# Kernel tuning notes

Measured on AMD Instinct MI355X. Metric: run time of the kernel, lower is better.

Reference implementation:

```python
import jax, jax.numpy as jnp
import numpy as np

B, L, PD, DIM, H, DH, DEPTH, MLP, NIMG, NCLS, TH = 2, 2048, 768, 512, 8, 64, 2, 2048, 4, 1000, 32


def _ln(x, g):
    # bias-free LayerNorm (beta buffer is zeros), eps matches torch F.layer_norm
    mu = jnp.mean(x, axis=-1, keepdims=True)
    var = jnp.var(x, axis=-1, keepdims=True)
    return (x - mu) / jnp.sqrt(var + 1e-5) * g


def _rms(x, g):
    # F.normalize(dim=-1) * sqrt(dim_head) * gamma; x: [b,h,n,dh], g: [h,1,dh]
    n = jnp.linalg.norm(x, axis=-1, keepdims=True)
    return x / jnp.maximum(n, 1e-12) * (DH ** 0.5) * g


def _attn(x, context, mask, ln_g, qg, kg, Wq, Wkv, Wo):
    b, n = x.shape[0], x.shape[1]
    xn = _ln(x, ln_g)
    kv = xn if context is None else context  # context is NOT pre-normed (matches source)
    m = kv.shape[1]
    q = (xn @ Wq).reshape(b, n, H, DH).transpose(0, 2, 1, 3)   # [b,h,n,dh]
    k, v = jnp.split(kv @ Wkv, 2, axis=-1)
    k = k.reshape(b, m, H, DH).transpose(0, 2, 1, 3)
    v = v.reshape(b, m, H, DH).transpose(0, 2, 1, 3)
    q = _rms(q, qg)
    k = _rms(k, kg)
    dots = jnp.einsum('bhid,bhjd->bhij', q, k)  # no 1/sqrt(d): QK-RMSNorm carries the scale
    neg = -jnp.finfo(dots.dtype).max
    dots = jnp.where(mask, dots, neg)
    a = jax.nn.softmax(dots, axis=-1)
    out = jnp.einsum('bhij,bhjd->bhid', a, v)
    out = out.transpose(0, 2, 1, 3).reshape(b, n, H * DH)
    return out @ Wo


def _forward(patches, ln_pe1_g, W_pe, b_pe, ln_pe2_g, pos_h_emb, pos_w_emb,
             attn_ln_g, q_g, k_g, Wq, Wkv, Wo, ff_ln_g, W1, b1, W2, b2,
             final_ln_g, pool_q, pool_ln_g, pool_q_g, pool_k_g,
             pool_Wq, pool_Wkv, pool_Wo, head_ln_g, W_head,
             pos_h, pos_w, image_ids):
    # patch embedding: LN -> Linear -> LN, then factorized 2D pos embed
    x = _ln(patches, ln_pe1_g) @ W_pe + b_pe
    x = _ln(x, ln_pe2_g)
    x = x + pos_h_emb[pos_h] + pos_w_emb[pos_w]
    # block-diagonal attention mask: tokens attend only within their image
    mask = (image_ids[:, None, :, None] == image_ids[:, None, None, :])  # [B,1,L,L]
    for i in range(DEPTH):
        x = _attn(x, None, mask, attn_ln_g[i], q_g[i], k_g[i], Wq[i], Wkv[i], Wo[i]) + x
        h = _ln(x, ff_ln_g[i]) @ W1[i] + b1[i]
        h = jax.nn.gelu(h, approximate=False)
        x = h @ W2[i] + b2[i] + x
    x = _ln(x, final_ln_g)
    # attention pooling: one learned query per packed image
    queries = jnp.broadcast_to(pool_q, (B, NIMG, DIM))
    pmask = (jnp.arange(NIMG)[None, None, :, None] == image_ids[:, None, None, :])  # [B,1,NIMG,L]
    pooled = _attn(queries, x, pmask, pool_ln_g, pool_q_g, pool_k_g, pool_Wq, pool_Wkv, pool_Wo) + queries
    return _ln(pooled, head_ln_g) @ W_head  # [B, NIMG, NCLS]


def setup_inputs() -> dict:
    key = jax.random.key(0)
    ks = jax.random.split(key, 16)
    s = 0.02
    inp = {}
    inp['patches'] = jax.random.normal(ks[0], (B, L, PD), jnp.float32)
    inp['pos_h'] = jax.random.randint(ks[1], (B, L), 0, TH)
    inp['pos_w'] = jax.random.randint(ks[2], (B, L), 0, TH)
    inp['image_ids'] = jnp.sort(jax.random.randint(ks[3], (B, L), 0, NIMG), axis=-1)
    inp['ln_pe1_g'] = jnp.ones((PD,), jnp.float32)
    inp['W_pe'] = jax.random.normal(ks[4], (PD, DIM), jnp.float32) * s
    inp['b_pe'] = jnp.zeros((DIM,), jnp.float32)
    inp['ln_pe2_g'] = jnp.ones((DIM,), jnp.float32)
    inp['pos_h_emb'] = jax.random.normal(ks[5], (TH, DIM), jnp.float32)
    inp['pos_w_emb'] = jax.random.normal(ks[6], (TH, DIM), jnp.float32)
    inp['attn_ln_g'] = jnp.ones((DEPTH, DIM), jnp.float32)
    inp['q_g'] = jnp.ones((DEPTH, H, 1, DH), jnp.float32)
    inp['k_g'] = jnp.ones((DEPTH, H, 1, DH), jnp.float32)
    inp['Wq'] = jax.random.normal(ks[7], (DEPTH, DIM, H * DH), jnp.float32) * s
    inp['Wkv'] = jax.random.normal(ks[8], (DEPTH, DIM, 2 * H * DH), jnp.float32) * s
    inp['Wo'] = jax.random.normal(ks[9], (DEPTH, H * DH, DIM), jnp.float32) * s
    inp['ff_ln_g'] = jnp.ones((DEPTH, DIM), jnp.float32)
    inp['W1'] = jax.random.normal(ks[10], (DEPTH, DIM, MLP), jnp.float32) * s
    inp['b1'] = jnp.zeros((DEPTH, MLP), jnp.float32)
    inp['W2'] = jax.random.normal(ks[11], (DEPTH, MLP, DIM), jnp.float32) * s
    inp['b2'] = jnp.zeros((DEPTH, DIM), jnp.float32)
    inp['final_ln_g'] = jnp.ones((DIM,), jnp.float32)
    inp['pool_q'] = jax.random.normal(ks[12], (DIM,), jnp.float32)
    inp['pool_ln_g'] = jnp.ones((DIM,), jnp.float32)
    inp['pool_q_g'] = jnp.ones((H, 1, DH), jnp.float32)
    inp['pool_k_g'] = jnp.ones((H, 1, DH), jnp.float32)
    inp['pool_Wq'] = jax.random.normal(ks[13], (DIM, H * DH), jnp.float32) * s
    inp['pool_Wkv'] = jax.random.normal(ks[14], (DIM, 2 * H * DH), jnp.float32) * s
    inp['pool_Wo'] = jax.random.normal(ks[15], (H * DH, DIM), jnp.float32) * s
    inp['head_ln_g'] = jnp.ones((DIM,), jnp.float32)
    inp['W_head'] = jax.random.normal(jax.random.fold_in(key, 99), (DIM, NCLS), jnp.float32) * s
    return inp


def reference(patches, pos_h, pos_w, image_ids, ln_pe1_g, W_pe, b_pe, ln_pe2_g,
              pos_h_emb, pos_w_emb, attn_ln_g, q_g, k_g, Wq, Wkv, Wo, ff_ln_g,
              W1, b1, W2, b2, final_ln_g, pool_q, pool_ln_g, pool_q_g, pool_k_g,
              pool_Wq, pool_Wkv, pool_Wo, head_ln_g, W_head):
    return _forward(patches, ln_pe1_g, W_pe, b_pe, ln_pe2_g, pos_h_emb, pos_w_emb,
                    attn_ln_g, q_g, k_g, Wq, Wkv, Wo, ff_ln_g, W1, b1, W2, b2,
                    final_ln_g, pool_q, pool_ln_g, pool_q_g, pool_k_g,
                    pool_Wq, pool_Wkv, pool_Wo, head_ln_g, W_head,
                    pos_h, pos_w, image_ids)
```

## Files before the change

### kernel.cpp

```cpp
#include <hip/hip_runtime.h>
#include <hip/hip_bf16.h>
#include <cfloat>
#include <math.h>

#define BB 2
#define LL 2048
#define PD 768
#define DIM 512
#define HH 8
#define DH 64
#define DEPTH 2
#define MLP 2048
#define NIMG 4
#define NCLS 1000
#define ROWS (BB*LL)
#define QKV (3*DIM)
#define NEGBIG (-1e30f)

typedef __hip_bfloat16 bf16;
typedef __bf16 v8bf __attribute__((ext_vector_type(8)));
typedef float f32x4 __attribute__((ext_vector_type(4)));

__device__ __forceinline__ float ldin(const void* p, size_t i, int bf) {
    return bf ? __bfloat162float(((const bf16*)p)[i]) : ((const float*)p)[i];
}
__device__ __forceinline__ float lda(const float* p, size_t i) { return p[i]; }
__device__ __forceinline__ float lda(const bf16* p, size_t i) { return __bfloat162float(p[i]); }
__device__ __forceinline__ void st(float* p, size_t i, float v) { p[i] = v; }
__device__ __forceinline__ void st(bf16* p, size_t i, float v) { p[i] = __float2bfloat16(v); }
__device__ __forceinline__ unsigned short f2bf(float x) {
    return __builtin_bit_cast(unsigned short, __float2bfloat16(x));
}
__device__ __forceinline__ float us2f(unsigned short u) {
    return __bfloat162float(__builtin_bit_cast(bf16, u));
}

__device__ __forceinline__ void stage16(const void* gsrc, void* ldst)
{
    __builtin_amdgcn_global_load_lds(
        (const __attribute__((address_space(1))) unsigned int*)(unsigned long long)gsrc,
        (__attribute__((address_space(3))) unsigned int*)(unsigned int)(unsigned long long)ldst,
        16, 0, 0);
}

__global__ void detect_dtype_kernel(const void* ones, int* flag)
{
    if (threadIdx.x == 0 && blockIdx.x == 0)
        *flag = (((const unsigned*)ones)[0] == 0x3F803F80u) ? 1 : 0;
}

__global__ void wconv_kernel(const void* __restrict__ W, int K, int N, size_t inStride,
                             bf16* __restrict__ out, size_t outOff, size_t outStride,
                             const int* dtf)
{
    __shared__ float t[32][33];
    const int bf = *dtf;
    const size_t zin = (size_t)blockIdx.z * inStride;
    const size_t zout = outOff + (size_t)blockIdx.z * outStride;
    const int kb = blockIdx.y * 32, nb = blockIdx.x * 32;
    const int tx = threadIdx.x, ty = threadIdx.y;
    #pragma unroll
    for (int u = 0; u < 4; ++u)
        t[ty + 8 * u][tx] = ldin(W, zin + (size_t)(kb + ty + 8 * u) * N + nb + tx, bf);
    __syncthreads();
    #pragma unroll
    for (int u = 0; u < 4; ++u)
        out[zout + (size_t)(nb + ty + 8 * u) * K + kb + tx] = __float2bfloat16(t[tx][ty + 8 * u]);
}

template<int RAWIN, typename TOUT>
__global__ void ln_kernel(const void* __restrict__ in, const void* __restrict__ g, size_t goff,
                          TOUT* __restrict__ out, int D, const int* dtf)
{
    __shared__ float red[16];
    const int bf = *dtf;
    const int row = blockIdx.x, tid = threadIdx.x;
    const size_t base = (size_t)row * D;
    float s = 0.f, ss = 0.f;
    for (int d = tid; d < D; d += blockDim.x) {
        float v = RAWIN ? ldin(in, base + d, bf) : ((const float*)in)[base + d];
        s += v; ss += v * v;
    }
    for (int o = 32; o; o >>= 1) { s += __shfl_xor(s, o); ss += __shfl_xor(ss, o); }
    const int wid = tid >> 6, lane = tid & 63, nw = blockDim.x >> 6;
    if (lane == 0) { red[wid] = s; red[8 + wid] = ss; }
    __syncthreads();
    if (tid == 0) {
        float a = 0.f, b = 0.f;
        for (int w = 0; w < nw; ++w) { a += red[w]; b += red[8 + w]; }
        red[0] = a; red[8] = b;
    }
    __syncthreads();
    const float mean = red[0] / D;
    const float var  = red[8] / D - mean * mean;
    const float rstd = rsqrtf(var + 1e-5f);
    for (int d = tid; d < D; d += blockDim.x) {
        float v = RAWIN ? ldin(in, base + d, bf) : ((const float*)in)[base + d];
        st(out, base + d, (v - mean) * rstd * ldin(g, goff + d, bf));
    }
}

__global__ void patch_fuse_kernel(const float* __restrict__ part,
                                  const void* __restrict__ b_pe,
                                  const void* __restrict__ g1,
                                  const void* __restrict__ phe, const void* __restrict__ pwe,
                                  const int* __restrict__ ph, const int* __restrict__ pw,
                                  const void* __restrict__ g2,
                                  float* __restrict__ x, bf16* __restrict__ xb,
                                  const int* dtf)
{
    __shared__ float red[16];
    const int bf = *dtf;
    const int row = blockIdx.x, tid = threadIdx.x;
    const size_t base = (size_t)row * DIM;
    const int wid = tid >> 6, lane = tid & 63;
    float v[2];
    float s = 0.f, ss = 0.f;
    #pragma unroll
    for (int u = 0; u < 2; ++u) {
        const int d = tid + 256 * u;
        float a = part[base + d] + part[(size_t)ROWS * DIM + base + d] + ldin(b_pe, d, bf);
        v[u] = a; s += a; ss += a * a;
    }
    for (int o = 32; o; o >>= 1) { s += __shfl_xor(s, o); ss += __shfl_xor(ss, o); }
    if (lane == 0) { red[wid] = s; red[8 + wid] = ss; }
    __syncthreads();
    if (tid == 0) {
        float a = 0.f, b = 0.f;
        for (int w2 = 0; w2 < 4; ++w2) { a += red[w2]; b += red[8 + w2]; }
        red[0] = a; red[8] = b;
    }
    __syncthreads();
    {
        const float mean = red[0] / DIM;
        const float var  = red[8] / DIM - mean * mean;
        const float rstd = rsqrtf(var + 1e-5f);
        const size_t hoff = (size_t)ph[row] * DIM, woff = (size_t)pw[row] * DIM;
        s = 0.f; ss = 0.f;
        #pragma unroll
        for (int u = 0; u < 2; ++u) {
            const int d = tid + 256 * u;
            float a = (v[u] - mean) * rstd * ldin(g1, d, bf)
                    + ldin(phe, hoff + d, bf) + ldin(pwe, woff + d, bf);
            x[base + d] = a;
            v[u] = a; s += a; ss += a * a;
        }
    }
    for (int o = 32; o; o >>= 1) { s += __shfl_xor(s, o); ss += __shfl_xor(ss, o); }
    __syncthreads();
    if (lane == 0) { red[wid] = s; red[8 + wid] = ss; }
    __syncthreads();
    if (tid == 0) {
        float a = 0.f, b = 0.f;
        for (int w2 = 0; w2 < 4; ++w2) { a += red[w2]; b += red[8 + w2]; }
        red[0] = a; red[8] = b;
    }
    __syncthreads();
    const float mean = red[0] / DIM;
    const float var  = red[8] / DIM - mean * mean;
    const float rstd = rsqrtf(var + 1e-5f);
    #pragma unroll
    for (int u = 0; u < 2; ++u) {
        const int d = tid + 256 * u;
        xb[base + d] = __float2bfloat16((v[u] - mean) * rstd * ldin(g2, d, bf));
    }
}

#define GM 128
#define GN 64
#define GK 64

template<typename TO, int EPI>
__global__ void mgemm_kernel(const bf16* __restrict__ A, const bf16* __restrict__ Wt,
                             const void* __restrict__ bias, size_t boff,
                             const float* __restrict__ resid, TO* __restrict__ out,
                             int M, int N, int K, int kc, int gelu, const int* dtf)
{
    __shared__ __align__(16) unsigned short As[GM][GK];
    __shared__ __align__(16) unsigned short Bs[GN][GK];
    const int tid = threadIdx.x;
    const int w = tid >> 6, l = tid & 63, g = l >> 4, c = l & 15;
    const int wm = (w >> 1) * 64, wn = (w & 1) * 32;
    const int m0 = blockIdx.y * GM, n0 = blockIdx.x * GN;
    const int kbeg = blockIdx.z * kc, kend = kbeg + kc;
    const int lrow = l >> 3, lcol = (l & 7) * 8;

    f32x4 acc[4][2] = {};

    for (int k0 = kbeg; k0 < kend; k0 += GK) {
        __syncthreads();
        #pragma unroll
        for (int u = 0; u < 4; ++u) {
            const int rr = 32 * w + 8 * u;
            stage16(A + (size_t)(m0 + rr + lrow) * K + k0 + lcol, &As[rr][0]);
        }
        #pragma unroll
        for (int u = 0; u < 2; ++u) {
            const int rr = 16 * w + 8 * u;
            stage16(Wt + (size_t)(n0 + rr + lrow) * K + k0 + lcol, &Bs[rr][0]);
        }
        __syncthreads();
        #pragma unroll
        for (int kk = 0; kk < GK; kk += 32) {
            v8bf av[4], bv[2];
            #pragma unroll
            for (int i = 0; i < 4; ++i) av[i] = *(const v8bf*)&As[wm + i * 16 + c][kk + 8 * g];
            #pragma unroll
            for (int j = 0; j < 2; ++j) bv[j] = *(const v8bf*)&Bs[wn + j * 16 + c][kk + 8 * g];
            #pragma unroll
            for (int i = 0; i < 4; ++i)
                #pragma unroll
                for (int j = 0; j < 2; ++j)
                    acc[i][j] = __builtin_amdgcn_mfma_f32_16x16x32_bf16(av[i], bv[j], acc[i][j], 0, 0, 0);
        }
    }

    if (EPI == 0) {
        float* po = (float*)out + (size_t)blockIdx.z * M * N;
        #pragma unroll
        for (int i = 0; i < 4; ++i) {
            const int rb = m0 + wm + i * 16 + 4 * g;
            #pragma unroll
            for (int j = 0; j < 2; ++j) {
                const int col = n0 + wn + j * 16 + c;
                #pragma unroll
                for (int r = 0; r < 4; ++r)
                    po[(size_t)(rb + r) * N + col] = acc[i][j][r];
            }
        }
    } else {
        const int bf = *dtf;
        #pragma unroll
        for (int i = 0; i < 4; ++i) {
            const int rb = m0 + wm + i * 16 + 4 * g;
            #pragma unroll
            for (int j = 0; j < 2; ++j) {
                const int col = n0 + wn + j * 16 + c;
                const float bvl = bias ? ldin(bias, boff + col, bf) : 0.f;
                #pragma unroll
                for (int r = 0; r < 4; ++r) {
                    float v = acc[i][j][r] + bvl;
                    if (gelu) v = 0.5f * v * (1.f + erff(v * 0.70710678118654752f));
                    if (resid) v += resid[(size_t)(rb + r) * N + col];
                    st(out, (size_t)(rb + r) * N + col, v);
                }
            }
        }
    }
}

__global__ void comb_ln_kernel(const float* __restrict__ part, int S,
                               const void* __restrict__ bias, size_t boff,
                               float* __restrict__ x, const void* __restrict__ g, size_t goff,
                               bf16* __restrict__ xb, const int* dtf)
{
    __shared__ float red[16];
    const int bf = *dtf;
    const int row = blockIdx.x, tid = threadIdx.x;
    const size_t base = (size_t)row * DIM;
    float v[2];
    float s = 0.f, ss = 0.f;
    #pragma unroll
    for (int u = 0; u < 2; ++u) {
        const int d = tid + 256 * u;
        float a = 0.f;
        for (int sc = 0; sc < S; ++sc) a += part[(size_t)sc * ROWS * DIM + base + d];
        if (bias) a += ldin(bias, boff + d, bf);
        a += x[base + d];
        x[base + d] = a;
        v[u] = a; s += a; ss += a * a;
    }
    for (int o = 32; o; o >>= 1) { s += __shfl_xor(s, o); ss += __shfl_xor(ss, o); }
    const int wid = tid >> 6, lane = tid & 63;
    if (lane == 0) { red[wid] = s; red[8 + wid] = ss; }
    __syncthreads();
    if (tid == 0) {
        float a = 0.f, b = 0.f;
        for (int w2 = 0; w2 < 4; ++w2) { a += red[w2]; b += red[8 + w2]; }
        red[0] = a; red[8] = b;
    }
    __syncthreads();
    const float mean = red[0] / DIM;
    const float var  = red[8] / DIM - mean * mean;
    const float rstd = rsqrtf(var + 1e-5f);
    #pragma unroll
    for (int u = 0; u < 2; ++u) {
        const int d = tid + 256 * u;
        xb[base + d] = __float2bfloat16((v[u] - mean) * rstd * ldin(g, goff + d, bf));
    }
}

#define TS 16
template<typename TA, typename TO>
__global__ void gemm_kernel(const TA* __restrict__ A, const void* __restrict__ W, size_t woff,
                            const void* __restrict__ bias, size_t boff,
                            const float* __restrict__ resid, TO* __restrict__ out,
                            int M, int N, int K, int gelu, const int* dtf)
{
    __shared__ float As[TS][TS + 1];
    __shared__ float Bs[TS][TS + 1];
    const int bf = *dtf;
    const int tx = threadIdx.x, ty = threadIdx.y;
    const int col = blockIdx.x * TS + tx;
    const int row = blockIdx.y * TS + ty;
    float acc = 0.f;
    for (int k0 = 0; k0 < K; k0 += TS) {
        const int ka = k0 + tx;
        As[ty][tx] = (row < M && ka < K) ? lda(A, (size_t)row * K + ka) : 0.f;
        const int kb = k0 + ty;
        Bs[ty][tx] = (col < N && kb < K) ? ldin(W, woff + (size_t)kb * N + col, bf) : 0.f;
        __syncthreads();
        #pragma unroll
        for (int kk = 0; kk < TS; ++kk) acc = fmaf(As[ty][kk], Bs[kk][tx], acc);
        __syncthreads();
    }
    if (row < M && col < N) {
        if (bias) acc += ldin(bias, boff + col, bf);
        if (gelu) acc = 0.5f * acc * (1.f + erff(acc * 0.70710678118654752f));
        if (resid) acc += resid[(size_t)row * N + col];
        st(out, (size_t)row * N + col, acc);
    }
}

__global__ void rms_kernel(float* __restrict__ buf, const void* __restrict__ g, size_t goff,
                           int stride, int colbase, const int* dtf)
{
    const int bf = *dtf;
    const int r = blockIdx.x, h = blockIdx.y, lane = threadIdx.x;
    float* p = buf + (size_t)r * stride + colbase + h * DH;
    const float v = p[lane];
    float ss = v * v;
    for (int o = 32; o; o >>= 1) ss += __shfl_xor(ss, o);
    const float norm = sqrtf(ss);
    const float sc = 8.0f / fmaxf(norm, 1e-12f);
    p[lane] = v * sc * ldin(g, goff + h * DH + lane, bf);
}

__global__ void rms2_kernel(bf16* __restrict__ buf, int stride,
                            const void* __restrict__ g0, size_t g0off,
                            int base1, const void* __restrict__ g1, size_t g1off,
                            int nslot, const int* dtf)
{
    const int bf = *dtf;
    const int tid = threadIdx.x;
    const int s = tid >> 4, li = tid & 15;
    if (s >= nslot) return;
    const int h = s & 7;
    const int colbase = (s < 8) ? 0 : base1;
    const void* g = (s < 8) ? g0 : g1;
    const size_t go = ((s < 8) ? g0off : g1off) + h * DH + li * 4;
    bf16* p = buf + (size_t)blockIdx.x * stride + colbase + h * DH + li * 4;
    ushort4 v = *(const ushort4*)p;
    const float f0 = us2f(v.x), f1 = us2f(v.y), f2 = us2f(v.z), f3 = us2f(v.w);
    float ss = f0 * f0 + f1 * f1 + f2 * f2 + f3 * f3;
    ss += __shfl_xor(ss, 8); ss += __shfl_xor(ss, 4);
    ss += __shfl_xor(ss, 2); ss += __shfl_xor(ss, 1);
    const float sc = 8.0f / fmaxf(sqrtf(ss), 1e-12f);
    ushort4 o;
    o.x = f2bf(f0 * sc * ldin(g, go + 0, bf));
    o.y = f2bf(f1 * sc * ldin(g, go + 1, bf));
    o.z = f2bf(f2 * sc * ldin(g, go + 2, bf));
    o.w = f2bf(f3 * sc * ldin(g, go + 3, bf));
    *(ushort4*)p = o;
}

#define QT 64
#define KT 64
#define LP 72

__global__ void flash_attn_kernel(const bf16* __restrict__ q, int qstr,
                                  const bf16* __restrict__ kpt, const bf16* __restrict__ vpt,
                                  int kvstr, const int* __restrict__ ids,
                                  bf16* __restrict__ out)
{
    __shared__ __align__(16) unsigned short Qs[QT][LP];
    __shared__ __align__(16) unsigned short Vt[DH][LP];
    __shared__ __align__(16) unsigned short Ps[QT][LP];
    __shared__ __align__(16) int ids_s[KT];
    __shared__ __align__(16) int qids_s[QT];
    __shared__ int range_s[2];

    const int tid = threadIdx.x;
    const int bid = blockIdx.x;
    const int s0 = (bid & 7) * 64 + (bid >> 3);
    const int qb = (s0 & 31) * QT;
    const int h = (s0 >> 5) & 7;
    const int b = s0 >> 8;
    const int w = tid >> 6, l = tid & 63, g = l >> 4, c = l & 15;

    {
        const int r = tid >> 2, c0 = (tid & 3) << 4;
        const bf16* qp = q + (size_t)(b * LL + qb + r) * qstr + h * DH + c0;
        *(int4*)&Qs[r][c0]     = *(const int4*)qp;
        *(int4*)&Qs[r][c0 + 8] = *(const int4*)(qp + 8);
        if (tid < QT) qids_s[tid] = ids[b * LL + qb + tid];
    }
    if (tid == 0) {
        const int* bp = ids + b * LL;
        const int qlo = bp[qb], qhi = bp[qb + QT - 1];
        int lo = 0, hi = LL;
        while (lo < hi) { int mid = (lo + hi) >> 1; if (bp[mid] < qlo) lo = mid + 1; else hi = mid; }
        range_s[0] = lo;
        int lo2 = 0, hi2 = LL;
        while (lo2 < hi2) { int mid = (lo2 + hi2) >> 1; if (bp[mid] <= qhi) lo2 = mid + 1; else hi2 = mid; }
        range_s[1] = lo2;
    }
    __syncthreads();

    const int myid = qids_s[16 * w + c];
    const v8bf qf0 = *(const v8bf*)&Qs[16 * w + c][8 * g];
    const v8bf qf1 = *(const v8bf*)&Qs[16 * w + c][8 * g + 32];
    const int kb_start = (range_s[0] / KT) * KT;
    const int kb_end = range_s[1];

    f32x4 o[4];
    #pragma unroll
    for (int dt = 0; dt < 4; ++dt) o[dt] = (f32x4){0.f, 0.f, 0.f, 0.f};
    float mr = NEGBIG, lr = 0.f;

    const int kp2 = (tid & 31) * 2, db = (tid >> 5) * 8;
    ushort4 va0, va1, vb0, vb1;
    int idv = 0;
    {
        const bf16* v0p = vpt + (size_t)(b * LL + kb_start + kp2) * kvstr + h * DH + db;
        const bf16* v1p = v0p + kvstr;
        va0 = *(const ushort4*)v0p; va1 = *(const ushort4*)(v0p + 4);
        vb0 = *(const ushort4*)v1p; vb1 = *(const ushort4*)(v1p + 4);
        if (tid < KT) idv = ids[b * LL + kb_start + tid];
    }

    for (int kb = kb_start; kb < kb_end; kb += KT) {
        __syncthreads();
        {
            const unsigned short* ap0 = (const unsigned short*)&va0;
            const unsigned short* ap1 = (const unsigned short*)&va1;
            const unsigned short* bp0 = (const unsigned short*)&vb0;
            const unsigned short* bp1 = (const unsigned short*)&vb1;
            #pragma unroll
            for (int j = 0; j < 4; ++j) {
                *(unsigned int*)&Vt[db + j][kp2]     = (unsigned)ap0[j] | ((unsigned)bp0[j] << 16);
                *(unsigned int*)&Vt[db + 4 + j][kp2] = (unsigned)ap1[j] | ((unsigned)bp1[j] << 16);
            }
            if (tid < KT) ids_s[tid] = idv;
        }
        if (kb + KT < kb_end) {
            const bf16* v0p = vpt + (size_t)(b * LL + kb + KT + kp2) * kvstr + h * DH + db;
            const bf16* v1p = v0p + kvstr;
            va0 = *(const ushort4*)v0p; va1 = *(const ushort4*)(v0p + 4);
            vb0 = *(const ushort4*)v1p; vb1 = *(const ushort4*)(v1p + 4);
            if (tid < KT) idv = ids[b * LL + kb + KT + tid];
        }
        asm volatile("s_waitcnt lgkmcnt(0)" ::: "memory");
        __builtin_amdgcn_s_barrier();
        __builtin_amdgcn_sched_barrier(0);

        const bf16* kbase = kpt + (size_t)(b * LL + kb) * kvstr + h * DH;
        f32x4 stt[4];
        #pragma unroll
        for (int t = 0; t < 4; ++t) {
            const bf16* kp = kbase + (size_t)(16 * t + c) * kvstr + 8 * g;
            v8bf kf0 = *(const v8bf*)kp;
            v8bf kf1 = *(const v8bf*)(kp + 32);
            stt[t] = (f32x4){0.f, 0.f, 0.f, 0.f};
            stt[t] = __builtin_amdgcn_mfma_f32_16x16x32_bf16(kf0, qf0, stt[t], 0, 0, 0);
            stt[t] = __builtin_amdgcn_mfma_f32_16x16x32_bf16(kf1, qf1, stt[t], 0, 0, 0);
        }

        float sv[16]; int mk[16];
        float tmax = NEGBIG;
        #pragma unroll
        for (int t = 0; t < 4; ++t) {
            int4 iv = *(const int4*)&ids_s[16 * t + 4 * g];
            const int* ivp = (const int*)&iv;
            #pragma unroll
            for (int r = 0; r < 4; ++r) {
                float s = stt[t][r];
                int m = (ivp[r] == myid);
                sv[4 * t + r] = s; mk[4 * t + r] = m;
                if (m) tmax = fmaxf(tmax, s);
            }
        }
        tmax = fmaxf(tmax, __shfl_xor(tmax, 16));
        tmax = fmaxf(tmax, __shfl_xor(tmax, 32));
        const float mnew = fmaxf(mr, tmax);
        const float al = __expf(mr - mnew);
        float tsum = 0.f;
        #pragma unroll
        for (int t = 0; t < 4; ++t) {
            ushort4 pk;
            unsigned short* pp = (unsigned short*)&pk;
            #pragma unroll
            for (int r = 0; r < 4; ++r) {
                float p = mk[4 * t + r] ? __expf(sv[4 * t + r] - mnew) : 0.f;
                tsum += p;
                pp[r] = f2bf(p);
            }
            *(ushort4*)&Ps[16 * w + c][16 * t + 4 * g] = pk;
        }
        tsum += __shfl_xor(tsum, 16);
        tsum += __shfl_xor(tsum, 32);
        lr = lr * al + tsum;
        mr = mnew;

        const float a0 = __shfl(al, 4 * g + 0);
        const float a1 = __shfl(al, 4 * g + 1);
        const float a2 = __shfl(al, 4 * g + 2);
        const float a3 = __shfl(al, 4 * g + 3);
        #pragma unroll
        for (int dt = 0; dt < 4; ++dt) {
            o[dt][0] *= a0; o[dt][1] *= a1; o[dt][2] *= a2; o[dt][3] *= a3;
        }

        const v8bf pf0 = *(const v8bf*)&Ps[16 * w + c][8 * g];
        const v8bf pf1 = *(const v8bf*)&Ps[16 * w + c][8 * g + 32];
        #pragma unroll
        for (int dt = 0; dt < 4; ++dt) {
            v8bf vf0 = *(const v8bf*)&Vt[16 * dt + c][8 * g];
            v8bf vf1 = *(const v8bf*)&Vt[16 * dt + c][8 * g + 32];
            o[dt] = __builtin_amdgcn_mfma_f32_16x16x32_bf16(pf0, vf0, o[dt], 0, 0, 0);
            o[dt] = __builtin_amdgcn_mfma_f32_16x16x32_bf16(pf1, vf1, o[dt], 0, 0, 0);
        }
    }

    const float li0 = 1.f / __shfl(lr, 4 * g + 0);
    const float li1 = 1.f / __shfl(lr, 4 * g + 1);
    const float li2 = 1.f / __shfl(lr, 4 * g + 2);
    const float li3 = 1.f / __shfl(lr, 4 * g + 3);
    #pragma unroll
    for (int dt = 0; dt < 4; ++dt) {
        bf16* op = out + (size_t)(b * LL + qb + 16 * w) * DIM + h * DH + 16 * dt + c;
        op[(size_t)(4 * g + 0) * DIM] = __float2bfloat16(o[dt][0] * li0);
        op[(size_t)(4 * g + 1) * DIM] = __float2bfloat16(o[dt][1] * li1);
        op[(size_t)(4 * g + 2) * DIM] = __float2bfloat16(o[dt][2] * li2);
        op[(size_t)(4 * g + 3) * DIM] = __float2bfloat16(o[dt][3] * li3);
    }
}

#define PCH 16
#define PCK (LL / PCH)

__global__ void pool_attn_part_kernel(const float* __restrict__ q, const bf16* __restrict__ kv,
                                      int kvs, const int* __restrict__ ids,
                                      float* __restrict__ ppm, float* __restrict__ ppl,
                                      float* __restrict__ ppo)
{
    const int iq = blockIdx.x & (NIMG - 1), ch = blockIdx.x >> 2;
    const int h = blockIdx.y, b = blockIdx.z;
    const int tid = threadIdx.x;
    const int qrow = b * NIMG + iq;
    const int j0 = ch * PCK;
    __shared__ float qs[DH];
    __shared__ float s[PCK];

    qs[tid] = q[(size_t)qrow * DIM + h * DH + tid];
    __syncthreads();
    #pragma unroll
    for (int u = 0; u < 2; ++u) {
        const int j = j0 + tid + 64 * u;
        const bf16* kp = kv + (size_t)(b * LL + j) * kvs + h * DH;
        float d = 0.f;
        #pragma unroll
        for (int t = 0; t < DH; t += 8) {
            int4 kvv = *(const int4*)&kp[t];
            const unsigned short* uu = (const unsigned short*)&kvv;
            #pragma unroll
            for (int z = 0; z < 8; ++z) d = fmaf(qs[t + z], us2f(uu[z]), d);
        }
        s[tid + 64 * u] = (ids[b * LL + j] == iq) ? d : NEGBIG;
    }
    __syncthreads();
    float m = fmaxf(s[tid], s[tid + 64]);
    for (int o = 32; o; o >>= 1) m = fmaxf(m, __shfl_xor(m, o));
    const float p0 = __expf(s[tid] - m), p1 = __expf(s[tid + 64] - m);
    float ls = p0 + p1;
    for (int o = 32; o; o >>= 1) ls += __shfl_xor(ls, o);
    s[tid] = p0; s[tid + 64] = p1;
    __syncthreads();
    float acc = 0.f;
    for (int jj = 0; jj < PCK; ++jj)
        acc += s[jj] * __bfloat162float(kv[(size_t)(b * LL + j0 + jj) * kvs + DIM + h * DH + tid]);
    const int p = ((b * HH + h) * NIMG + iq) * PCH + ch;
    if (tid == 0) { ppm[p] = m; ppl[p] = ls; }
    ppo[(size_t)p * DH + tid] = acc;
}

__global__ void pool_attn_comb_kernel(const float* __restrict__ ppm, const float* __restrict__ ppl,
                                      const float* __restrict__ ppo, float* __restrict__ out)
{
    const int iq = blockIdx.x, h = blockIdx.y, b = blockIdx.z;
    const int d = threadIdx.x;
    const int pb = ((b * HH + h) * NIMG + iq) * PCH;
    float mstar = NEGBIG;
    #pragma unroll
    for (int ch = 0; ch < PCH; ++ch) mstar = fmaxf(mstar, ppm[pb + ch]);
    float lsum = 0.f, osum = 0.f;
    #pragma unroll
    for (int ch = 0; ch < PCH; ++ch) {
        const float w = __expf(ppm[pb + ch] - mstar);
        lsum += ppl[pb + ch] * w;
        osum += ppo[(size_t)(pb + ch) * DH + d] * w;
    }
    out[(size_t)(b * NIMG + iq) * DIM + h * DH + d] = osum / lsum;
}

__global__ void fill_q_kernel(float* __restrict__ queries, const void* __restrict__ pool_q,
                              const int* dtf)
{
    const int bf = *dtf;
    const int idx = blockIdx.x * blockDim.x + threadIdx.x;
    if (idx < BB * NIMG * DIM) queries[idx] = ldin(pool_q, idx % DIM, bf);
}

__global__ void write_out_kernel(const float* __restrict__ in, void* __restrict__ out, int n,
                                 const int* dtf)
{
    const int bf = *dtf;
    const int idx = blockIdx.x * blockDim.x + threadIdx.x;
    if (idx < n) {
        if (bf) ((bf16*)out)[idx] = __float2bfloat16(in[idx]);
        else    ((float*)out)[idx] = in[idx];
    }
}

extern "C" void kernel_launch(void* const* d_in, const int* in_sizes, int n_in,
                              void* d_out, int out_size, void* d_ws, size_t ws_size,
                              hipStream_t stream)
{
    const void* patches   = d_in[0];
    const int*  pos_h     = (const int*) d_in[1];
    const int*  pos_w     = (const int*) d_in[2];
    const int*  image_ids = (const int*) d_in[3];
    const void* ln_pe1_g  = d_in[4];
    const void* W_pe      = d_in[5];
    const void* b_pe      = d_in[6];
    const void* ln_pe2_g  = d_in[7];
    const void* pos_h_emb = d_in[8];
    const void* pos_w_emb = d_in[9];
    const void* attn_ln_g = d_in[10];
    const void* q_g       = d_in[11];
    const void* k_g       = d_in[12];
    const void* Wq        = d_in[13];
    const void* Wkv       = d_in[14];
    const void* Wo        = d_in[15];
    const void* ff_ln_g   = d_in[16];
    const void* W1        = d_in[17];
    const void* b1        = d_in[18];
    const void* W2        = d_in[19];
    const void* b2        = d_in[20];
    const void* final_ln_g= d_in[21];
    const void* pool_q    = d_in[22];
    const void* pool_ln_g = d_in[23];
    const void* pool_q_g  = d_in[24];
    const void* pool_k_g  = d_in[25];
    const void* pool_Wq   = d_in[26];
    const void* pool_Wkv  = d_in[27];
    const void* pool_Wo   = d_in[28];
    const void* head_ln_g = d_in[29];
    const void* W_head    = d_in[30];

    char* p = (char*)d_ws;
    int* flag = (int*)p;                         p += 256;
    float* x   = (float*)p;                      p += (size_t)ROWS * DIM * 4;
    bf16* xb   = (bf16*)p;                       p += (size_t)ROWS * PD * 2;
    bf16* qkvb = (bf16*)p;  bf16* hb = qkvb;     p += (size_t)ROWS * MLP * 2;
    bf16* wpeT  = (bf16*)p;                      p += (size_t)DIM * PD * 2;
    bf16* wqkvT = (bf16*)p;                      p += (size_t)DEPTH * QKV * DIM * 2;
    bf16* woT   = (bf16*)p;                      p += (size_t)DEPTH * DIM * DIM * 2;
    bf16* w1T   = (bf16*)p;                      p += (size_t)DEPTH * MLP * DIM * 2;
    bf16* w2T   = (bf16*)p;                      p += (size_t)DEPTH * DIM * MLP * 2;
    bf16* pkvT  = (bf16*)p;                      p += (size_t)2 * DIM * DIM * 2;
    float* queries = (float*)p;                  p += 4096 * 4;
    float* qp      = (float*)p;                  p += 4096 * 4;
    float* pattn   = (float*)p;                  p += 4096 * 4;
    float* pooled  = (float*)p;                  p += 4096 * 4;
    bf16*  pln     = (bf16*)p;                   p += 4096 * 2;
    float* hout    = (float*)p;                  p += 8192 * 4;
    float* ppm     = (float*)p;                  p += 1024 * 4;
    float* ppl     = (float*)p;                  p += 1024 * 4;
    float* ppo     = (float*)p;                  p += (size_t)1024 * DH * 4;
    float* part    = (float*)p;                  p += (size_t)4 * ROWS * DIM * 4;

    const dim3 blk256(256);
    const dim3 blkG(TS, TS);
    const dim3 blkT(32, 8);

    detect_dtype_kernel<<<1, 1, 0, stream>>>(ln_pe1_g, flag);

    wconv_kernel<<<dim3(DIM / 32, PD / 32, 1), blkT, 0, stream>>>(
        W_pe, PD, DIM, 0, wpeT, 0, 0, flag);
    wconv_kernel<<<dim3(DIM / 32, DIM / 32, DEPTH), blkT, 0, stream>>>(
        Wq, DIM, DIM, (size_t)DIM * DIM, wqkvT, 0, (size_t)QKV * DIM, flag);
    wconv_kernel<<<dim3(2 * DIM / 32, DIM / 32, DEPTH), blkT, 0, stream>>>(
        Wkv, DIM, 2 * DIM, (size_t)DIM * 2 * DIM, wqkvT, (size_t)DIM * DIM, (size_t)QKV * DIM, flag);
    wconv_kernel<<<dim3(DIM / 32, DIM / 32, DEPTH), blkT, 0, stream>>>(
        Wo, DIM, DIM, (size_t)DIM * DIM, woT, 0, (size_t)DIM * DIM, flag);
    wconv_kernel<<<dim3(MLP / 32, DIM / 32, DEPTH), blkT, 0, stream>>>(
        W1, DIM, MLP, (size_t)DIM * MLP, w1T, 0, (size_t)MLP * DIM, flag);
    wconv_kernel<<<dim3(DIM / 32, MLP / 32, DEPTH), blkT, 0, stream>>>(
        W2, MLP, DIM, (size_t)MLP * DIM, w2T, 0, (size_t)DIM * MLP, flag);
    wconv_kernel<<<dim3(2 * DIM / 32, DIM / 32, 1), blkT, 0, stream>>>(
        pool_Wkv, DIM, 2 * DIM, 0, pkvT, 0, 0, flag);

    ln_kernel<1, bf16><<<ROWS, blk256, 0, stream>>>(patches, ln_pe1_g, 0, xb, PD, flag);
    mgemm_kernel<float, 0><<<dim3(DIM / GN, ROWS / GM, 2), blk256, 0, stream>>>(
        xb, wpeT, nullptr, 0, nullptr, part, ROWS, DIM, PD, PD / 2, 0, flag);
    patch_fuse_kernel<<<ROWS, blk256, 0, stream>>>(
        part, b_pe, ln_pe2_g, pos_h_emb, pos_w_emb, pos_h, pos_w, attn_ln_g, x, xb, flag);

    for (int i = 0; i < DEPTH; ++i) {
        mgemm_kernel<bf16, 1><<<dim3(QKV / GN, ROWS / GM, 1), blk256, 0, stream>>>(
            xb, wqkvT + (size_t)i * QKV * DIM, nullptr, 0, nullptr, qkvb,
            ROWS, QKV, DIM, DIM, 0, flag);
        rms2_kernel<<<ROWS, blk256, 0, stream>>>(
            qkvb, QKV, q_g, (size_t)i * HH * DH, DIM, k_g, (size_t)i * HH * DH, 16, flag);
        flash_attn_kernel<<<dim3(512), blk256, 0, stream>>>(
            qkvb, QKV, qkvb + DIM, qkvb + 2 * DIM, QKV, image_ids, xb);
        mgemm_kernel<float, 0><<<dim3(DIM / GN, ROWS / GM, 2), blk256, 0, stream>>>(
            xb, woT + (size_t)i * DIM * DIM, nullptr, 0, nullptr, part,
            ROWS, DIM, DIM, DIM / 2, 0, flag);
        comb_ln_kernel<<<ROWS, blk256, 0, stream>>>(
            part, 2, nullptr, 0, x, ff_ln_g, (size_t)i * DIM, xb, flag);
        mgemm_kernel<bf16, 1><<<dim3(MLP / GN, ROWS / GM, 1), blk256, 0, stream>>>(
            xb, w1T + (size_t)i * MLP * DIM, b1, (size_t)i * MLP, nullptr, hb,
            ROWS, MLP, DIM, DIM, 1, flag);
        mgemm_kernel<float, 0><<<dim3(DIM / GN, ROWS / GM, 4), blk256, 0, stream>>>(
            hb, w2T + (size_t)i * DIM * MLP, nullptr, 0, nullptr, part,
            ROWS, DIM, MLP, MLP / 4, 0, flag);
        const void* gnext = (i + 1 < DEPTH) ? attn_ln_g : final_ln_g;
        const size_t gnoff = (i + 1 < DEPTH) ? (size_t)(i + 1) * DIM : 0;
        comb_ln_kernel<<<ROWS, blk256, 0, stream>>>(
            part, 4, b2, (size_t)i * DIM, x, gnext, gnoff, xb, flag);
    }

    fill_q_kernel<<<(BB * NIMG * DIM + 255) / 256, blk256, 0, stream>>>(queries, pool_q, flag);
    ln_kernel<0, bf16><<<BB * NIMG, blk256, 0, stream>>>(queries, pool_ln_g, 0, pln, DIM, flag);
    gemm_kernel<bf16, float><<<dim3(DIM / TS, 1), blkG, 0, stream>>>(
        pln, pool_Wq, 0, nullptr, 0, nullptr, qp, BB * NIMG, DIM, DIM, 0, flag);
    mgemm_kernel<bf16, 1><<<dim3(2 * DIM / GN, ROWS / GM, 1), blk256, 0, stream>>>(
        xb, pkvT, nullptr, 0, nullptr, qkvb, ROWS, 2 * DIM, DIM, DIM, 0, flag);
    rms_kernel<<<dim3(BB * NIMG, HH), dim3(64), 0, stream>>>(
        qp, pool_q_g, 0, DIM, 0, flag);
    rms2_kernel<<<ROWS, blk256, 0, stream>>>(
        qkvb, 2 * DIM, pool_k_g, 0, 0, nullptr, 0, 8, flag);
    pool_attn_part_kernel<<<dim3(NIMG * PCH, HH, BB), dim3(64), 0, stream>>>(
        qp, qkvb, 2 * DIM, image_ids, ppm, ppl, ppo);
    pool_attn_comb_kernel<<<dim3(NIMG, HH, BB), dim3(64), 0, stream>>>(ppm, ppl, ppo, pattn);
    gemm_kernel<float, float><<<dim3(DIM / TS, 1), blkG, 0, stream>>>(
        pattn, pool_Wo, 0, nullptr, 0, queries, pooled, BB * NIMG, DIM, DIM, 0, flag);

    ln_kernel<0, bf16><<<BB * NIMG, blk256, 0, stream>>>(pooled, head_ln_g, 0, pln, DIM, flag);
    gemm_kernel<bf16, float><<<dim3((NCLS + TS - 1) / TS, 1), blkG, 0, stream>>>(
        pln, W_head, 0, nullptr, 0, nullptr, hout, BB * NIMG, NCLS, DIM, 0, flag);
    write_out_kernel<<<(BB * NIMG * NCLS + 255) / 256, blk256, 0, stream>>>(
        hout, d_out, BB * NIMG * NCLS, flag);
}
```

Before: 495.4 us.

## Fuse QK RMSNorm into flash attention and double-buffer GEMM LDS tiles

Removes the separate rms2 kernel and instead normalizes Q when loading it and normalizes each K tile inside the attention loop, staging K through shared memory rather than reading it directly from global memory. The V register prefetch is dropped, and MFMA sections get s_setprio hints. The GEMM gets double-buffered LDS staging with explicit vmcnt waits so the next tile loads while the current one computes. In exchange, K is renormalized by every query block that reads it, shared memory usage grows, and the V/id prefetch overlap is lost.

After: 463.8 us. 6.4% less time.

```diff
diff --git a/kernel.cpp b/kernel.cpp
--- a/kernel.cpp
+++ b/kernel.cpp
@@ -176,44 +176,59 @@
                              const float* __restrict__ resid, TO* __restrict__ out,
                              int M, int N, int K, int kc, int gelu, const int* dtf)
 {
-    __shared__ __align__(16) unsigned short As[GM][GK];
-    __shared__ __align__(16) unsigned short Bs[GN][GK];
+    __shared__ __align__(16) unsigned short As[2][GM][GK];
+    __shared__ __align__(16) unsigned short Bs[2][GN][GK];
     const int tid = threadIdx.x;
     const int w = tid >> 6, l = tid & 63, g = l >> 4, c = l & 15;
     const int wm = (w >> 1) * 64, wn = (w & 1) * 32;
     const int m0 = blockIdx.y * GM, n0 = blockIdx.x * GN;
-    const int kbeg = blockIdx.z * kc, kend = kbeg + kc;
+    const int kbeg = blockIdx.z * kc;
     const int lrow = l >> 3, lcol = (l & 7) * 8;
 
+#define STAGE_MG(BUF, K0)                                                          \
+    {                                                                              \
+        _Pragma("unroll")                                                          \
+        for (int u = 0; u < 4; ++u) {                                              \
+            const int rr = 32 * w + 8 * u;                                         \
+            stage16(A + (size_t)(m0 + rr + lrow) * K + (K0) + lcol, &As[BUF][rr][0]); \
+        }                                                                          \
+        _Pragma("unroll")                                                          \
+        for (int u = 0; u < 2; ++u) {                                              \
+            const int rr = 16 * w + 8 * u;                                         \
+            stage16(Wt + (size_t)(n0 + rr + lrow) * K + (K0) + lcol, &Bs[BUF][rr][0]); \
+        }                                                                          \
+    }
+
     f32x4 acc[4][2] = {};
-
-    for (int k0 = kbeg; k0 < kend; k0 += GK) {
-        __syncthreads();
-        #pragma unroll
-        for (int u = 0; u < 4; ++u) {
-            const int rr = 32 * w + 8 * u;
-            stage16(A + (size_t)(m0 + rr + lrow) * K + k0 + lcol, &As[rr][0]);
-        }
-        #pragma unroll
-        for (int u = 0; u < 2; ++u) {
-            const int rr = 16 * w + 8 * u;
-            stage16(Wt + (size_t)(n0 + rr + lrow) * K + k0 + lcol, &Bs[rr][0]);
-        }
-        __syncthreads();
+    const int nt = kc / GK;
+    STAGE_MG(0, kbeg);
+    int cur = 0;
+    for (int t = 0; t < nt; ++t) {
+        if (t + 1 < nt) {
+            STAGE_MG(cur ^ 1, kbeg + (t + 1) * GK);
+            asm volatile("s_waitcnt vmcnt(6)" ::: "memory");
+        } else {
+            asm volatile("s_waitcnt vmcnt(0)" ::: "memory");
+        }
+        __builtin_amdgcn_s_barrier();
+        __builtin_amdgcn_sched_barrier(0);
         #pragma unroll
         for (int kk = 0; kk < GK; kk += 32) {
             v8bf av[4], bv[2];
             #pragma unroll
-            for (int i = 0; i < 4; ++i) av[i] = *(const v8bf*)&As[wm + i * 16 + c][kk + 8 * g];
-            #pragma unroll
-            for (int j = 0; j < 2; ++j) bv[j] = *(const v8bf*)&Bs[wn + j * 16 + c][kk + 8 * g];
+            for (int i = 0; i < 4; ++i) av[i] = *(const v8bf*)&As[cur][wm + i * 16 + c][kk + 8 * g];
+            #pragma unroll
+            for (int j = 0; j < 2; ++j) bv[j] = *(const v8bf*)&Bs[cur][wn + j * 16 + c][kk + 8 * g];
             #pragma unroll
             for (int i = 0; i < 4; ++i)
                 #pragma unroll
                 for (int j = 0; j < 2; ++j)
                     acc[i][j] = __builtin_amdgcn_mfma_f32_16x16x32_bf16(av[i], bv[j], acc[i][j], 0, 0, 0);
         }
-    }
+        __builtin_amdgcn_s_barrier();
+        cur ^= 1;
+    }
+#undef STAGE_MG
 
     if (EPI == 0) {
         float* po = (float*)out + (size_t)blockIdx.z * M * N;
@@ -371,15 +386,18 @@
 __global__ void flash_attn_kernel(const bf16* __restrict__ q, int qstr,
                                   const bf16* __restrict__ kpt, const bf16* __restrict__ vpt,
                                   int kvstr, const int* __restrict__ ids,
-                                  bf16* __restrict__ out)
+                                  const void* __restrict__ qg, const void* __restrict__ kg,
+                                  size_t goff, bf16* __restrict__ out, const int* dtf)
 {
     __shared__ __align__(16) unsigned short Qs[QT][LP];
+    __shared__ __align__(16) unsigned short Ks[KT][LP];
     __shared__ __align__(16) unsigned short Vt[DH][LP];
     __shared__ __align__(16) unsigned short Ps[QT][LP];
     __shared__ __align__(16) int ids_s[KT];
     __shared__ __align__(16) int qids_s[QT];
     __shared__ int range_s[2];
 
+    const int bf = *dtf;
     const int tid = threadIdx.x;
     const int bid = blockIdx.x;
     const int s0 = (bid & 7) * 64 + (bid >> 3);
@@ -388,11 +406,35 @@
     const int b = s0 >> 8;
     const int w = tid >> 6, l = tid & 63, g = l >> 4, c = l & 15;
 
+    const int r4 = tid >> 2, c16 = (tid & 3) << 4;
+
+    float gk[16];
+    #pragma unroll
+    for (int j = 0; j < 16; ++j) gk[j] = ldin(kg, goff + h * DH + c16 + j, bf);
+
     {
-        const int r = tid >> 2, c0 = (tid & 3) << 4;
-        const bf16* qp = q + (size_t)(b * LL + qb + r) * qstr + h * DH + c0;
-        *(int4*)&Qs[r][c0]     = *(const int4*)qp;
-        *(int4*)&Qs[r][c0 + 8] = *(const int4*)(qp + 8);
+        const bf16* qp = q + (size_t)(b * LL + qb + r4) * qstr + h * DH + c16;
+        int4 raw0 = *(const int4*)qp;
+        int4 raw1 = *(const int4*)(qp + 8);
+        const unsigned short* u0 = (const unsigned short*)&raw0;
+        const unsigned short* u1 = (const unsigned short*)&raw1;
+        float f[16];
+        float ssq = 0.f;
+        #pragma unroll
+        for (int j = 0; j < 8; ++j) { f[j] = us2f(u0[j]); f[8 + j] = us2f(u1[j]); }
+        #pragma unroll
+        for (int j = 0; j < 16; ++j) ssq += f[j] * f[j];
+        ssq += __shfl_xor(ssq, 1); ssq += __shfl_xor(ssq, 2);
+        const float sc = 8.0f / fmaxf(sqrtf(ssq), 1e-12f);
+        ushort4 pk[4];
+        unsigned short* pp = (unsigned short*)pk;
+        #pragma unroll
+        for (int j = 0; j < 16; ++j)
+            pp[j] = f2bf(f[j] * sc * ldin(qg, goff + h * DH + c16 + j, bf));
+        *(ushort4*)&Qs[r4][c16]      = pk[0];
+        *(ushort4*)&Qs[r4][c16 + 4]  = pk[1];
+        *(ushort4*)&Qs[r4][c16 + 8]  = pk[2];
+        *(ushort4*)&Qs[r4][c16 + 12] = pk[3];
         if (tid < QT) qids_s[tid] = ids[b * LL + qb + tid];
     }
     if (tid == 0) {
@@ -418,53 +460,63 @@
     for (int dt = 0; dt < 4; ++dt) o[dt] = (f32x4){0.f, 0.f, 0.f, 0.f};
     float mr = NEGBIG, lr = 0.f;
 
-    const int kp2 = (tid & 31) * 2, db = (tid >> 5) * 8;
-    ushort4 va0, va1, vb0, vb1;
-    int idv = 0;
-    {
-        const bf16* v0p = vpt + (size_t)(b * LL + kb_start + kp2) * kvstr + h * DH + db;
-        const bf16* v1p = v0p + kvstr;
-        va0 = *(const ushort4*)v0p; va1 = *(const ushort4*)(v0p + 4);
-        vb0 = *(const ushort4*)v1p; vb1 = *(const ushort4*)(v1p + 4);
-        if (tid < KT) idv = ids[b * LL + kb_start + tid];
-    }
-
     for (int kb = kb_start; kb < kb_end; kb += KT) {
         __syncthreads();
         {
-            const unsigned short* ap0 = (const unsigned short*)&va0;
-            const unsigned short* ap1 = (const unsigned short*)&va1;
-            const unsigned short* bp0 = (const unsigned short*)&vb0;
-            const unsigned short* bp1 = (const unsigned short*)&vb1;
+            const bf16* kp = kpt + (size_t)(b * LL + kb + r4) * kvstr + h * DH + c16;
+            int4 raw0 = *(const int4*)kp;
+            int4 raw1 = *(const int4*)(kp + 8);
+            const unsigned short* u0 = (const unsigned short*)&raw0;
+            const unsigned short* u1 = (const unsigned short*)&raw1;
+            float f[16];
+            float ssq = 0.f;
+            #pragma unroll
+            for (int j = 0; j < 8; ++j) { f[j] = us2f(u0[j]); f[8 + j] = us2f(u1[j]); }
+            #pragma unroll
+            for (int j = 0; j < 16; ++j) ssq += f[j] * f[j];
+            ssq += __shfl_xor(ssq, 1); ssq += __shfl_xor(ssq, 2);
+            const float sc = 8.0f / fmaxf(sqrtf(ssq), 1e-12f);
+            ushort4 pk[4];
+            unsigned short* pp = (unsigned short*)pk;
+            #pragma unroll
+            for (int j = 0; j < 16; ++j) pp[j] = f2bf(f[j] * sc * gk[j]);
+            *(ushort4*)&Ks[r4][c16]      = pk[0];
+            *(ushort4*)&Ks[r4][c16 + 4]  = pk[1];
+            *(ushort4*)&Ks[r4][c16 + 8]  = pk[2];
+            *(ushort4*)&Ks[r4][c16 + 12] = pk[3];
+        }
+        {
+            const int kp2 = (tid & 31) * 2, db = (tid >> 5) * 8;
+            const bf16* v0p = vpt + (size_t)(b * LL + kb + kp2) * kvstr + h * DH + db;
+            const bf16* v1p = v0p + kvstr;
+            const ushort4 a0 = *(const ushort4*)v0p;
+            const ushort4 a1 = *(const ushort4*)(v0p + 4);
+            const ushort4 b0 = *(const ushort4*)v1p;
+            const ushort4 b1 = *(const ushort4*)(v1p + 4);
+            const unsigned short* ap0 = (const unsigned short*)&a0;
+            const unsigned short* ap1 = (const unsigned short*)&a1;
+            const unsigned short* bp0 = (const unsigned short*)&b0;
+            const unsigned short* bp1 = (const unsigned short*)&b1;
             #pragma unroll
             for (int j = 0; j < 4; ++j) {
                 *(unsigned int*)&Vt[db + j][kp2]     = (unsigned)ap0[j] | ((unsigned)bp0[j] << 16);
                 *(unsigned int*)&Vt[db + 4 + j][kp2] = (unsigned)ap1[j] | ((unsigned)bp1[j] << 16);
             }
-            if (tid < KT) ids_s[tid] = idv;
-        }
-        if (kb + KT < kb_end) {
-            const bf16* v0p = vpt + (size_t)(b * LL + kb + KT + kp2) * kvstr + h * DH + db;
-            const bf16* v1p = v0p + kvstr;
-            va0 = *(const ushort4*)v0p; va1 = *(const ushort4*)(v0p + 4);
-            vb0 = *(const ushort4*)v1p; vb1 = *(const ushort4*)(v1p + 4);
-            if (tid < KT) idv = ids[b * LL + kb + KT + tid];
-        }
-        asm volatile("s_waitcnt lgkmcnt(0)" ::: "memory");
-        __builtin_amdgcn_s_barrier();
-        __builtin_amdgcn_sched_barrier(0);
-
-        const bf16* kbase = kpt + (size_t)(b * LL + kb) * kvstr + h * DH;
+        }
+        if (tid < KT) ids_s[tid] = ids[b * LL + kb + tid];
+        __syncthreads();
+
         f32x4 stt[4];
+        __builtin_amdgcn_s_setprio(1);
         #pragma unroll
         for (int t = 0; t < 4; ++t) {
-            const bf16* kp = kbase + (size_t)(16 * t + c) * kvstr + 8 * g;
-            v8bf kf0 = *(const v8bf*)kp;
-            v8bf kf1 = *(const v8bf*)(kp + 32);
             stt[t] = (f32x4){0.f, 0.f, 0.f, 0.f};
+            v8bf kf0 = *(const v8bf*)&Ks[16 * t + c][8 * g];
+            v8bf kf1 = *(const v8bf*)&Ks[16 * t + c][8 * g + 32];
             stt[t] = __builtin_amdgcn_mfma_f32_16x16x32_bf16(kf0, qf0, stt[t], 0, 0, 0);
             stt[t] = __builtin_amdgcn_mfma_f32_16x16x32_bf16(kf1, qf1, stt[t], 0, 0, 0);
         }
+        __builtin_amdgcn_s_setprio(0);
 
         float sv[16]; int mk[16];
         float tmax = NEGBIG;
@@ -513,6 +565,7 @@
 
         const v8bf pf0 = *(const v8bf*)&Ps[16 * w + c][8 * g];
         const v8bf pf1 = *(const v8bf*)&Ps[16 * w + c][8 * g + 32];
+        __builtin_amdgcn_s_setprio(1);
         #pragma unroll
         for (int dt = 0; dt < 4; ++dt) {
             v8bf vf0 = *(const v8bf*)&Vt[16 * dt + c][8 * g];
@@ -520,6 +573,7 @@
             o[dt] = __builtin_amdgcn_mfma_f32_16x16x32_bf16(pf0, vf0, o[dt], 0, 0, 0);
             o[dt] = __builtin_amdgcn_mfma_f32_16x16x32_bf16(pf1, vf1, o[dt], 0, 0, 0);
         }
+        __builtin_amdgcn_s_setprio(0);
     }
 
     const float li0 = 1.f / __shfl(lr, 4 * g + 0);
@@ -711,10 +765,9 @@
         mgemm_kernel<bf16, 1><<<dim3(QKV / GN, ROWS / GM, 1), blk256, 0, stream>>>(
             xb, wqkvT + (size_t)i * QKV * DIM, nullptr, 0, nullptr, qkvb,
             ROWS, QKV, DIM, DIM, 0, flag);
-        rms2_kernel<<<ROWS, blk256, 0, stream>>>(
-            qkvb, QKV, q_g, (size_t)i * HH * DH, DIM, k_g, (size_t)i * HH * DH, 16, flag);
         flash_attn_kernel<<<dim3(512), blk256, 0, stream>>>(
-            qkvb, QKV, qkvb + DIM, qkvb + 2 * DIM, QKV, image_ids, xb);
+            qkvb, QKV, qkvb + DIM, qkvb + 2 * DIM, QKV, image_ids,
+            q_g, k_g, (size_t)i * HH * DH, xb, flag);
         mgemm_kernel<float, 0><<<dim3(DIM / GN, ROWS / GM, 2), blk256, 0, stream>>>(
             xb, woT + (size_t)i * DIM * DIM, nullptr, 0, nullptr, part,
             ROWS, DIM, DIM, DIM / 2, 0, flag);
```
